# Performance work log

Measured on AMD Instinct MI355X. Metric: run time of the kernel, lower is better.

Reference implementation:

```python
import jax, jax.numpy as jnp
import numpy as np

IN_FEATURES = 128
OUT_FEATURES = 128
GRID_SIZE = 5
SPLINE_ORDER = 3
N_KNOTS = GRID_SIZE + 2 * SPLINE_ORDER + 1  # 12
N_BASIS = GRID_SIZE + SPLINE_ORDER          # 8


def b_spline_basis(x, grid, spline_order):
    # x: [N, in], grid: [in, n_knots] -> basis: [N, in, n_basis]
    xe = x[..., None]
    basis = ((xe >= grid[..., :-1]) & (xe < grid[..., 1:])).astype(x.dtype)
    for k in range(1, spline_order + 1):
        left = (xe - grid[..., :-(k + 1)]) / (grid[..., k:-1] - grid[..., :-(k + 1)] + 1e-08)
        right = (grid[..., k + 1:] - xe) / (grid[..., k + 1:] - grid[..., 1:-k] + 1e-08)
        basis = left * basis[..., :-1] + right * basis[..., 1:]
    return basis


def setup_inputs() -> dict:
    key = jax.random.key(0)
    k_x, k_bw, k_sw = jax.random.split(key, 3)
    x = jax.random.normal(k_x, (16, 4096, IN_FEATURES), dtype=jnp.float32)
    grid = jnp.tile(jnp.linspace(-1.0, 1.0, N_KNOTS, dtype=jnp.float32)[None, :], (IN_FEATURES, 1))
    base_weight = jax.random.normal(k_bw, (OUT_FEATURES, IN_FEATURES), dtype=jnp.float32) * 0.1
    base_bias = jnp.zeros((OUT_FEATURES,), dtype=jnp.float32)
    spline_weight = jax.random.normal(k_sw, (OUT_FEATURES, IN_FEATURES, N_BASIS), dtype=jnp.float32) * 0.1
    spline_bias = jnp.zeros((OUT_FEATURES,), dtype=jnp.float32)
    spline_scale = jnp.ones((1,), dtype=jnp.float32)
    return {"x": x, "grid": grid, "base_weight": base_weight, "base_bias": base_bias,
            "spline_weight": spline_weight, "spline_bias": spline_bias, "spline_scale": spline_scale}


def reference(x, grid, base_weight, base_bias, spline_weight, spline_bias, spline_scale):
    orig_shape = x.shape
    x_flat = x.reshape(-1, IN_FEATURES)                      # [N, in]
    base_out = jax.nn.silu(x_flat) @ base_weight.T + base_bias  # [N, out]
    x_norm = jnp.tanh(x_flat)
    basis = b_spline_basis(x_norm, grid, SPLINE_ORDER)       # [N, in, n_basis]
    spline_out = jnp.einsum('oib,nib->no', spline_weight, basis) + spline_bias
    out = base_out + spline_scale * spline_out
    return out.reshape(*orig_shape[:-1], OUT_FEATURES)
```

## Files before the change

### kernel.cpp

```cpp
#include <hip/hip_runtime.h>
#include <hip/hip_bf16.h>


typedef __attribute__((ext_vector_type(8))) short short8;
typedef __attribute__((ext_vector_type(4))) float f32x4;
typedef __attribute__((ext_vector_type(4))) unsigned int u32x4;
typedef __attribute__((ext_vector_type(8))) unsigned short u16x8;

#define GLOAD_LDS16(g, l) __builtin_amdgcn_global_load_lds(                 \
    (const __attribute__((address_space(1))) void*)(g),                     \
    (__attribute__((address_space(3))) void*)(l), 16, 0, 0)

__device__ __forceinline__ unsigned short f2bf(float f) {
    unsigned u = __builtin_bit_cast(unsigned, f);
    return (unsigned short)((u + 0x7fffu + ((u >> 16) & 1u)) >> 16);
}
__device__ __forceinline__ unsigned pack_bf2(float lo, float hi) {
    unsigned a = __builtin_bit_cast(unsigned, lo) + 0x8000u;
    unsigned b = __builtin_bit_cast(unsigned, hi) + 0x8000u;
    return __builtin_amdgcn_perm(b, a, 0x07060302u);
}
__device__ __forceinline__ float fexp2(float f) { return __builtin_amdgcn_exp2f(f); }
__device__ __forceinline__ float frcp(float f)  { return __builtin_amdgcn_rcpf(f); }
__device__ __forceinline__ float fsilu(float v) {
    return v * frcp(1.0f + fexp2(v * -1.442695041f));
}

__device__ __forceinline__ short8 spline_frag(float xv) {
    float e  = fexp2(xv * 2.885390082f);
    float r  = frcp(1.0f + e);
    float t  = __builtin_fmaf(-2.0f, r, 1.0f);
    float u  = __builtin_fmaf(t, 5.5f, 5.5f);
    int   j  = (int)u;
    float w  = u - (float)j;
    float w2 = w * w;
    float omw = 1.0f - w;
    float v1 = __builtin_fmaf(__builtin_fmaf(0.5f, w, -1.0f), w2, 0.66666667f);
    float v2 = __builtin_fmaf(__builtin_fmaf(__builtin_fmaf(-0.5f, w, 0.5f), w, 0.5f), w,
                              0.16666667f);
    float om2 = omw * omw;
    float v0 = (om2 * 0.16666667f) * omw;
    float v3 = (w * 0.16666667f) * w2;
    unsigned P01 = pack_bf2(v0, v1);
    unsigned P23 = pack_bf2(v2, v3);
    unsigned long long P = (unsigned long long)P01 | ((unsigned long long)P23 << 32);
    int s = (j - 3) << 4;
    unsigned long long lo, hi;
    lo = (s >= 0) ? ((s < 64) ? (P << s) : 0ull) : (P >> (-s));
    hi = (s <= 0) ? 0ull
                  : ((s < 64) ? (P >> (64 - s))
                              : ((s < 128) ? (P << (s - 64)) : 0ull));
    u32x4 f = { (unsigned)lo, (unsigned)(lo >> 32), (unsigned)hi, (unsigned)(hi >> 32) };
    return __builtin_bit_cast(short8, f);
}

__global__ void kan_prep(const float* __restrict__ spline_w,
                         const float* __restrict__ base_w,
                         const float* __restrict__ scale_p,
                         unsigned short* __restrict__ wpre) {
    int g   = blockIdx.x * 256 + threadIdx.x;
    int p   = g >> 11;
    int rem = g & 2047;
    int o   = rem >> 4;
    int k0  = (rem & 15) << 3;
    const float* src = (p < 8) ? (spline_w + (o << 10) + (p << 7) + k0)
                               : (base_w + (o << 7) + k0);
    float s = (p < 8) ? scale_p[0] : 1.0f;
    float4 a = *(const float4*)(src);
    float4 b = *(const float4*)(src + 4);
    u16x8 pk = { f2bf(a.x * s), f2bf(a.y * s), f2bf(a.z * s), f2bf(a.w * s),
                 f2bf(b.x * s), f2bf(b.y * s), f2bf(b.z * s), f2bf(b.w * s) };
    unsigned byte = (unsigned)(((o << 8) + (k0 << 1)) ^ ((o & 7) << 4));
    *(u16x8*)((char*)wpre + (p << 15) + byte) = pk;
}

__global__ __launch_bounds__(256, 2) void kan_main(
    const float* __restrict__ x,
    const unsigned short* __restrict__ wpre,
    const float* __restrict__ base_b,
    const float* __restrict__ spline_b,
    const float* __restrict__ scale_p,
    float* __restrict__ out)
{
    __shared__ unsigned short lds_w[2 * 128 * 128];

    const int tid  = threadIdx.x;
    const int lane = tid & 63;
    const int wave = tid >> 6;
    const int l15  = lane & 15;
    const int kb   = lane >> 4;
    const int row0 = (int)blockIdx.x * 128;

    f32x4 acc[2][8];
#pragma unroll
    for (int m = 0; m < 2; ++m)
#pragma unroll
        for (int n = 0; n < 8; ++n) acc[m][n] = (f32x4){0.f, 0.f, 0.f, 0.f};

    char* lwbase = (char*)lds_w;
    const char* wsrc = (const char*)wpre;

    const float* xp0 = x + (row0 + (wave << 5) + l15) * 128 + kb;
    const float* xp1 = xp0 + 16 * 128;

    {
        const char* src = wsrc + (wave << 13) + (lane << 4);
        char* dst = lwbase + (wave << 13);
#pragma unroll
        for (int it = 0; it < 8; ++it) GLOAD_LDS16(src + (it << 10), dst + (it << 10));
    }
    float xs[2][4], xsn[2][4];
#pragma unroll
    for (int ks = 0; ks < 4; ++ks) { xs[0][ks] = xp0[ks << 2]; xs[1][ks] = xp1[ks << 2]; }
    __syncthreads();

    float4 xb[2][4][2];

    for (int p = 0; p < 8; ++p) {
        char* cur = lwbase + ((p & 1) << 15);
        char* nxt = lwbase + (((p + 1) & 1) << 15);

        {
            const char* src = wsrc + ((p + 1) << 15) + (wave << 13) + (lane << 4);
            char* dst = nxt + (wave << 13);
#pragma unroll
            for (int it = 0; it < 8; ++it) GLOAD_LDS16(src + (it << 10), dst + (it << 10));
        }
        if (p < 7) {
            const int c = (p + 1) << 4;
#pragma unroll
            for (int ks = 0; ks < 4; ++ks) {
                xsn[0][ks] = xp0[c + (ks << 2)];
                xsn[1][ks] = xp1[c + (ks << 2)];
            }
        } else {
            const float* xq0 = x + (row0 + (wave << 5) + l15) * 128 + (kb << 3);
            const float* xq1 = xq0 + 16 * 128;
#pragma unroll
            for (int ks = 0; ks < 4; ++ks) {
                xb[0][ks][0] = *(const float4*)(xq0 + (ks << 5));
                xb[0][ks][1] = *(const float4*)(xq0 + (ks << 5) + 4);
                xb[1][ks][0] = *(const float4*)(xq1 + (ks << 5));
                xb[1][ks][1] = *(const float4*)(xq1 + (ks << 5) + 4);
            }
        }

        short8 af[2][4];
#pragma unroll
        for (int m = 0; m < 2; ++m)
#pragma unroll
            for (int ks = 0; ks < 4; ++ks) af[m][ks] = spline_frag(xs[m][ks]);
        if (p < 7) {
#pragma unroll
            for (int m = 0; m < 2; ++m)
#pragma unroll
                for (int ks = 0; ks < 4; ++ks) xs[m][ks] = xsn[m][ks];
        }

#pragma unroll
        for (int ks = 0; ks < 4; ++ks) {
            short8 bfr[8];
#pragma unroll
            for (int n = 0; n < 8; ++n) {
                int o = (n << 4) + l15;
                unsigned byte = (unsigned)(((o << 8) + (ks << 6) + (kb << 4)) ^ ((o & 7) << 4));
                bfr[n] = *(const short8*)(cur + byte);
            }
#pragma unroll
            for (int m = 0; m < 2; ++m)
#pragma unroll
                for (int n = 0; n < 8; ++n)
                    acc[m][n] = __builtin_amdgcn_mfma_f32_16x16x32_bf16(
                        af[m][ks], bfr[n], acc[m][n], 0, 0, 0);
        }
        __syncthreads();
    }

    {
        char* cur = lwbase;
        short8 af[2][4];
#pragma unroll
        for (int m = 0; m < 2; ++m)
#pragma unroll
            for (int ks = 0; ks < 4; ++ks) {
                float4 a0 = xb[m][ks][0], a1 = xb[m][ks][1];
                u32x4 f = { pack_bf2(fsilu(a0.x), fsilu(a0.y)),
                            pack_bf2(fsilu(a0.z), fsilu(a0.w)),
                            pack_bf2(fsilu(a1.x), fsilu(a1.y)),
                            pack_bf2(fsilu(a1.z), fsilu(a1.w)) };
                af[m][ks] = __builtin_bit_cast(short8, f);
            }
#pragma unroll
        for (int ks = 0; ks < 4; ++ks) {
            short8 bfr[8];
#pragma unroll
            for (int n = 0; n < 8; ++n) {
                int o = (n << 4) + l15;
                unsigned byte = (unsigned)(((o << 8) + (ks << 6) + (kb << 4)) ^ ((o & 7) << 4));
                bfr[n] = *(const short8*)(cur + byte);
            }
#pragma unroll
            for (int m = 0; m < 2; ++m)
#pragma unroll
                for (int n = 0; n < 8; ++n)
                    acc[m][n] = __builtin_amdgcn_mfma_f32_16x16x32_bf16(
                        af[m][ks], bfr[n], acc[m][n], 0, 0, 0);
        }
    }

    const float scale = scale_p[0];
    float* ob = out + (row0 + (wave << 5) + (kb << 2)) * 128 + l15;
#pragma unroll
    for (int n = 0; n < 8; ++n) {
        int o = (n << 4) + l15;
        float bias = base_b[o] + scale * spline_b[o];
#pragma unroll
        for (int m = 0; m < 2; ++m) {
            float* obm = ob + (m << 4) * 128 + (n << 4);
#pragma unroll
            for (int j = 0; j < 4; ++j)
                obm[j * 128] = acc[m][n][j] + bias;
        }
    }
}

extern "C" void kernel_launch(void* const* d_in, const int* in_sizes, int n_in,
                              void* d_out, int out_size, void* d_ws, size_t ws_size,
                              hipStream_t stream) {
    const float* x  = (const float*)d_in[0];
    const float* bw = (const float*)d_in[2];
    const float* bb = (const float*)d_in[3];
    const float* sw = (const float*)d_in[4];
    const float* sb = (const float*)d_in[5];
    const float* sc = (const float*)d_in[6];
    float* out = (float*)d_out;

    unsigned short* wpre = (unsigned short*)d_ws;
    hipLaunchKernelGGL(kan_prep, dim3(72), dim3(256), 0, stream, sw, bw, sc, wpre);

    int nrows   = in_sizes[0] / 128;
    int nblocks = nrows / 128;
    hipLaunchKernelGGL(kan_main, dim3(nblocks), dim3(256), 0, stream,
                       x, wpre, bb, sb, sc, out);
}
```

Before: 44.14 us.

## Split kan_main work across 8 waves with 2x4 M/N wave tiling

Doubles the block to 512 threads and splits each 32-row slice between two waves that each own half of the 128 output columns, so each wave holds half as many accumulators and does half the B-fragment LDS reads per k-step. The weight prefetch is spread over 8 waves, and the base-path x loads move from the last spline iteration to just before the SiLU stage to save registers. The aim is more waves in flight for latency hiding. The cost is that every x row's spline basis is now computed twice, once by each N-half wave, and the base-path x load is no longer overlapped with the final spline iteration.

```diff
diff --git a/kernel.cpp b/kernel.cpp
--- a/kernel.cpp
+++ b/kernel.cpp
@@ -74,7 +74,7 @@
     *(u16x8*)((char*)wpre + (p << 15) + byte) = pk;
 }
 
-__global__ __launch_bounds__(256, 2) void kan_main(
+__global__ __launch_bounds__(512, 4) void kan_main(
     const float* __restrict__ x,
     const unsigned short* __restrict__ wpre,
     const float* __restrict__ base_b,
@@ -87,44 +87,44 @@
     const int tid  = threadIdx.x;
     const int lane = tid & 63;
     const int wave = tid >> 6;
+    const int wm   = wave >> 1;
+    const int wn   = wave & 1;
     const int l15  = lane & 15;
     const int kb   = lane >> 4;
     const int row0 = (int)blockIdx.x * 128;
 
-    f32x4 acc[2][8];
+    f32x4 acc[2][4];
 #pragma unroll
     for (int m = 0; m < 2; ++m)
 #pragma unroll
-        for (int n = 0; n < 8; ++n) acc[m][n] = (f32x4){0.f, 0.f, 0.f, 0.f};
+        for (int n = 0; n < 4; ++n) acc[m][n] = (f32x4){0.f, 0.f, 0.f, 0.f};
 
     char* lwbase = (char*)lds_w;
     const char* wsrc = (const char*)wpre;
 
-    const float* xp0 = x + (row0 + (wave << 5) + l15) * 128 + kb;
+    const float* xp0 = x + (row0 + (wm << 5) + l15) * 128 + kb;
     const float* xp1 = xp0 + 16 * 128;
 
     {
-        const char* src = wsrc + (wave << 13) + (lane << 4);
-        char* dst = lwbase + (wave << 13);
-#pragma unroll
-        for (int it = 0; it < 8; ++it) GLOAD_LDS16(src + (it << 10), dst + (it << 10));
+        const char* src = wsrc + (wave << 12) + (lane << 4);
+        char* dst = lwbase + (wave << 12);
+#pragma unroll
+        for (int it = 0; it < 4; ++it) GLOAD_LDS16(src + (it << 10), dst + (it << 10));
     }
     float xs[2][4], xsn[2][4];
 #pragma unroll
     for (int ks = 0; ks < 4; ++ks) { xs[0][ks] = xp0[ks << 2]; xs[1][ks] = xp1[ks << 2]; }
     __syncthreads();
-
-    float4 xb[2][4][2];
 
     for (int p = 0; p < 8; ++p) {
         char* cur = lwbase + ((p & 1) << 15);
         char* nxt = lwbase + (((p + 1) & 1) << 15);
 
         {
-            const char* src = wsrc + ((p + 1) << 15) + (wave << 13) + (lane << 4);
-            char* dst = nxt + (wave << 13);
-#pragma unroll
-            for (int it = 0; it < 8; ++it) GLOAD_LDS16(src + (it << 10), dst + (it << 10));
+            const char* src = wsrc + ((p + 1) << 15) + (wave << 12) + (lane << 4);
+            char* dst = nxt + (wave << 12);
+#pragma unroll
+            for (int it = 0; it < 4; ++it) GLOAD_LDS16(src + (it << 10), dst + (it << 10));
         }
         if (p < 7) {
             const int c = (p + 1) << 4;
@@ -133,16 +133,6 @@
                 xsn[0][ks] = xp0[c + (ks << 2)];
                 xsn[1][ks] = xp1[c + (ks << 2)];
             }
-        } else {
-            const float* xq0 = x + (row0 + (wave << 5) + l15) * 128 + (kb << 3);
-            const float* xq1 = xq0 + 16 * 128;
-#pragma unroll
-            for (int ks = 0; ks < 4; ++ks) {
-                xb[0][ks][0] = *(const float4*)(xq0 + (ks << 5));
-                xb[0][ks][1] = *(const float4*)(xq0 + (ks << 5) + 4);
-                xb[1][ks][0] = *(const float4*)(xq1 + (ks << 5));
-                xb[1][ks][1] = *(const float4*)(xq1 + (ks << 5) + 4);
-            }
         }
 
         short8 af[2][4];
@@ -159,17 +149,17 @@
 
 #pragma unroll
         for (int ks = 0; ks < 4; ++ks) {
-            short8 bfr[8];
-#pragma unroll
-            for (int n = 0; n < 8; ++n) {
-                int o = (n << 4) + l15;
+            short8 bfr[4];
+#pragma unroll
+            for (int n = 0; n < 4; ++n) {
+                int o = (wn << 6) + (n << 4) + l15;
                 unsigned byte = (unsigned)(((o << 8) + (ks << 6) + (kb << 4)) ^ ((o & 7) << 4));
                 bfr[n] = *(const short8*)(cur + byte);
             }
 #pragma unroll
             for (int m = 0; m < 2; ++m)
 #pragma unroll
-                for (int n = 0; n < 8; ++n)
+                for (int n = 0; n < 4; ++n)
                     acc[m][n] = __builtin_amdgcn_mfma_f32_16x16x32_bf16(
                         af[m][ks], bfr[n], acc[m][n], 0, 0, 0);
         }
@@ -178,41 +168,47 @@
 
     {
         char* cur = lwbase;
-        short8 af[2][4];
-#pragma unroll
-        for (int m = 0; m < 2; ++m)
-#pragma unroll
-            for (int ks = 0; ks < 4; ++ks) {
-                float4 a0 = xb[m][ks][0], a1 = xb[m][ks][1];
+#pragma unroll
+        for (int m = 0; m < 2; ++m) {
+            const float* xq = x + (row0 + (wm << 5) + (m << 4) + l15) * 128 + (kb << 3);
+            float4 xa[4][2];
+#pragma unroll
+            for (int ks = 0; ks < 4; ++ks) {
+                xa[ks][0] = *(const float4*)(xq + (ks << 5));
+                xa[ks][1] = *(const float4*)(xq + (ks << 5) + 4);
+            }
+            short8 af[4];
+#pragma unroll
+            for (int ks = 0; ks < 4; ++ks) {
+                float4 a0 = xa[ks][0], a1 = xa[ks][1];
                 u32x4 f = { pack_bf2(fsilu(a0.x), fsilu(a0.y)),
                             pack_bf2(fsilu(a0.z), fsilu(a0.w)),
                             pack_bf2(fsilu(a1.x), fsilu(a1.y)),
                             pack_bf2(fsilu(a1.z), fsilu(a1.w)) };
-                af[m][ks] = __builtin_bit_cast(short8, f);
-            }
-#pragma unroll
-        for (int ks = 0; ks < 4; ++ks) {
-            short8 bfr[8];
-#pragma unroll
-            for (int n = 0; n < 8; ++n) {
-                int o = (n << 4) + l15;
-                unsigned byte = (unsigned)(((o << 8) + (ks << 6) + (kb << 4)) ^ ((o & 7) << 4));
-                bfr[n] = *(const short8*)(cur + byte);
-            }
-#pragma unroll
-            for (int m = 0; m < 2; ++m)
-#pragma unroll
-                for (int n = 0; n < 8; ++n)
+                af[ks] = __builtin_bit_cast(short8, f);
+            }
+#pragma unroll
+            for (int ks = 0; ks < 4; ++ks) {
+                short8 bfr[4];
+#pragma unroll
+                for (int n = 0; n < 4; ++n) {
+                    int o = (wn << 6) + (n << 4) + l15;
+                    unsigned byte = (unsigned)(((o << 8) + (ks << 6) + (kb << 4)) ^ ((o & 7) << 4));
+                    bfr[n] = *(const short8*)(cur + byte);
+                }
+#pragma unroll
+                for (int n = 0; n < 4; ++n)
                     acc[m][n] = __builtin_amdgcn_mfma_f32_16x16x32_bf16(
-                        af[m][ks], bfr[n], acc[m][n], 0, 0, 0);
+                        af[ks], bfr[n], acc[m][n], 0, 0, 0);
+            }
         }
     }
 
     const float scale = scale_p[0];
-    float* ob = out + (row0 + (wave << 5) + (kb << 2)) * 128 + l15;
-#pragma unroll
-    for (int n = 0; n < 8; ++n) {
-        int o = (n << 4) + l15;
+    float* ob = out + (row0 + (wm << 5) + (kb << 2)) * 128 + (wn << 6) + l15;
+#pragma unroll
+    for (int n = 0; n < 4; ++n) {
+        int o = (wn << 6) + (n << 4) + l15;
         float bias = base_b[o] + scale * spline_b[o];
 #pragma unroll
         for (int m = 0; m < 2; ++m) {
@@ -240,6 +236,6 @@
 
     int nrows   = in_sizes[0] / 128;
     int nblocks = nrows / 128;
-    hipLaunchKernelGGL(kan_main, dim3(nblocks), dim3(256), 0, stream,
+    hipLaunchKernelGGL(kan_main, dim3(nblocks), dim3(512), 0, stream,
                        x, wpre, bb, sb, sc, out);
 }
```

Measured after the change: 63.17 us. +43.1%, slower.
